# Kernel optimization log

Measured on AMD Instinct MI355X. Metric: run time of the kernel, lower is better.

The kernel has to match this reference:

```python
import jax, jax.numpy as jnp
import numpy as np

DIM, K, B, H, W = 256, 7, 16, 56, 56
EPS = 1e-5

def _conv(x, w, pad, groups=1):
    return jax.lax.conv_general_dilated(
        x, w, window_strides=(1, 1), padding=[(pad, pad), (pad, pad)],
        dimension_numbers=('NCHW', 'OIHW', 'NCHW'), feature_group_count=groups)

def _bn(x, g, b, m, v):
    scale = g / jnp.sqrt(v + EPS)          # [C]
    bias = b - m * scale
    return x * scale[None, :, None, None] + bias[None, :, None, None]

def _silu(x):
    return x * jax.nn.sigmoid(x)

def setup_inputs() -> dict:
    key = jax.random.key(0)
    ks = jax.random.split(key, 12)
    f = lambda k_, shp, s=0.05: jax.random.normal(k_, shp, jnp.float32) * s
    d = {
        'x':   jax.random.normal(ks[0], (B, DIM, H, W), jnp.float32),
        # RepConv branch: dense 3x3 conv + BN, dense 1x1 conv + BN
        'w3':  f(ks[1], (DIM, DIM, 3, 3)),
        'g1':  1.0 + f(ks[2], (DIM,)), 'b1': f(ks[3], (DIM,)),
        'm1':  f(ks[4], (DIM,)),       'v1': jax.random.uniform(ks[4], (DIM,), jnp.float32) + 0.5,
        'w1':  f(ks[5], (DIM, DIM, 1, 1)),
        'g2':  1.0 + f(ks[6], (DIM,)), 'b2': f(ks[7], (DIM,)),
        'm2':  f(ks[8], (DIM,)),       'v2': jax.random.uniform(ks[8], (DIM,), jnp.float32) + 0.5,
        # depthwise branches
        'dw7': f(ks[9], (DIM, 1, 7, 7)),
        'dwk': f(ks[10], (DIM, 1, K, K)),
        # final BN
        'g3':  1.0 + f(ks[11], (DIM,)), 'b3': f(ks[11], (DIM,)),
        'm3':  f(ks[11], (DIM,)),       'v3': jax.random.uniform(ks[11], (DIM,), jnp.float32) + 0.5,
    }
    return d

def reference(x, w3, g1, b1, m1, v1, w1, g2, b2, m2, v2, dw7, dwk, g3, b3, m3, v3):
    # RepConv (train-mode, bn=False): SiLU(BN(conv3x3(x)) + BN(conv1x1(x)))
    rep = _silu(_bn(_conv(x, w3, 1), g1, b1, m1, v1)
                + _bn(_conv(x, w1, 0), g2, b2, m2, v2))
    # parallel depthwise branches
    y = rep + _conv(x, dw7, 3, groups=DIM) + _conv(x, dwk, K // 2, groups=DIM)
    return _silu(_bn(y, g3, b3, m3, v3))
```

## Files before the change

kernel.cpp:

```cpp
#include <hip/hip_runtime.h>
#include <stdint.h>
#include <stddef.h>

#define DIM 256
#define NB 16
#define HH 56
#define WW 56
#define HWP (HH*WW)
#define PH 62
#define PW 62
#define NPIX (NB*HWP)
#define EPSV 1e-5f

using f32x4  = __attribute__((ext_vector_type(4))) float;
using bf16x8 = __attribute__((ext_vector_type(8))) __bf16;

static __device__ __forceinline__ unsigned short f2bf(float f) {
    union { float f; unsigned u; } v; v.f = f;
    unsigned r = v.u + 0x7FFFu + ((v.u >> 16) & 1u);
    return (unsigned short)(r >> 16);
}
static __device__ __forceinline__ float bf2f(unsigned short u) {
    union { unsigned u; float f; } v; v.u = ((unsigned)u) << 16; return v.f;
}
static __device__ __forceinline__ float silu_f(float z) {
    return z / (1.f + __expf(-z));
}

__global__ __launch_bounds__(256)
void fused_prep(const float* __restrict__ x,
                const float* __restrict__ w3, const float* __restrict__ g1,
                const float* __restrict__ b1, const float* __restrict__ m1,
                const float* __restrict__ v1, const float* __restrict__ w1,
                const float* __restrict__ g2, const float* __restrict__ b2,
                const float* __restrict__ m2, const float* __restrict__ v2,
                const float* __restrict__ dw7, const float* __restrict__ dwk,
                const float* __restrict__ g3, const float* __restrict__ b3,
                const float* __restrict__ m3, const float* __restrict__ v3,
                unsigned short* __restrict__ xpad, unsigned short* __restrict__ WkT,
                unsigned short* __restrict__ dwout, float* __restrict__ biasm,
                float* __restrict__ sc3, float* __restrict__ bi3)
{
    __shared__ float shbuf[PH*64];
    int bid = blockIdx.x;
    int t = threadIdx.x;

    if (bid < 4096) {
        float (*plane)[64] = (float(*)[64])shbuf;
        int c = bid & 255, b = bid >> 8;
#pragma unroll
        for (int j = 0; j < 4; ++j) {
            int idx = j*256 + t;
            if (idx < 992) ((f32x4*)plane)[idx] = (f32x4){0.f,0.f,0.f,0.f};
        }
        __syncthreads();
        const float* xp = x + ((size_t)b*DIM + c)*HWP;
#pragma unroll
        for (int j = 0; j < 13; ++j) {
            int idx = j*256 + t;
            if (idx < HWP) {
                int h = idx / 56, w = idx % 56;
                plane[h + 3][w + 3] = xp[idx];
            }
        }
        float wr[49];
#pragma unroll
        for (int i = 0; i < 49; ++i) wr[i] = dw7[c*49 + i] + dwk[c*49 + i];
        __syncthreads();
        unsigned short* op = dwout + ((size_t)b*DIM + c)*HWP;
#pragma unroll
        for (int j = 0; j < 2; ++j) {
            int q = j*256 + t;
            if (q < 392) {
                int h = q / 7, w0 = (q % 7)*8;
                float a[8] = {0.f,0.f,0.f,0.f,0.f,0.f,0.f,0.f};
#pragma unroll
                for (int dy = 0; dy < 7; ++dy) {
                    const float* row = &plane[h + dy][w0];
                    union { f32x4 v[4]; float s[16]; } rr;
                    rr.v[0] = *(const f32x4*)(row);
                    rr.v[1] = *(const f32x4*)(row + 4);
                    rr.v[2] = *(const f32x4*)(row + 8);
                    rr.v[3] = *(const f32x4*)(row + 12);
#pragma unroll
                    for (int dx = 0; dx < 7; ++dx) {
                        float wv = wr[dy*7 + dx];
#pragma unroll
                        for (int o = 0; o < 8; ++o) a[o] += rr.s[dx + o] * wv;
                    }
                }
                uint4 pk;
                pk.x = (unsigned)f2bf(a[0]) | ((unsigned)f2bf(a[1]) << 16);
                pk.y = (unsigned)f2bf(a[2]) | ((unsigned)f2bf(a[3]) << 16);
                pk.z = (unsigned)f2bf(a[4]) | ((unsigned)f2bf(a[5]) << 16);
                pk.w = (unsigned)f2bf(a[6]) | ((unsigned)f2bf(a[7]) << 16);
                *(uint4*)&op[h*WW + w0] = pk;
            }
        }
        return;
    }

    if (bid < 8064) {
        float (*lds)[57] = (float(*)[57])shbuf;
        int idx0 = bid - 4096;
        int cc = idx0 & 3;
        int r62 = (idx0 >> 2);
        int ph = r62 % PH, b = r62 / PH;
        int c0 = cc*64;
        char* rowc = (char*)xpad + ((size_t)(b*PH + ph)*PW)*(DIM*2) + c0*2;

        if (ph < 3 || ph >= HH + 3) {
            uint4 z = {0u,0u,0u,0u};
#pragma unroll
            for (int j = 0; j < 2; ++j) {
                int idx = j*256 + t;
                if (idx < 496) {
                    int pix = idx >> 3, q = idx & 7;
                    *(uint4*)(rowc + (size_t)pix*(DIM*2) + q*16) = z;
                }
            }
            return;
        }
        if (t < 48) {
            int p = t >> 3, q = t & 7;
            int pw = (p < 3) ? p : (PW - 6 + p);
            uint4 z = {0u,0u,0u,0u};
            *(uint4*)(rowc + (size_t)pw*(DIM*2) + q*16) = z;
        }
        int h = ph - 3;
#pragma unroll
        for (int j = 0; j < 14; ++j) {
            int idx = j*256 + t;
            int c = idx / 56, w = idx % 56;
            lds[c][w] = x[((size_t)(b*DIM + c0 + c)*HH + h)*WW + w];
        }
        __syncthreads();
#pragma unroll
        for (int j = 0; j < 7; ++j) {
            int idx = j*256 + t;
            int w = idx >> 5, cp = idx & 31;
            unsigned lo = f2bf(lds[2*cp][w]);
            unsigned hi = f2bf(lds[2*cp+1][w]);
            unsigned val = lo | (hi << 16);
            *(unsigned*)(rowc + (size_t)(w + 3)*(DIM*2) + 4*cp) = val;
        }
        return;
    }

    {
        int co = bid - 8064;
        float s1 = g1[co] * rsqrtf(v1[co] + EPSV);
        float s2 = g2[co] * rsqrtf(v2[co] + EPSV);
        float w1v = w1[co*DIM + t] * s2;
        const float* w3r = w3 + (size_t)(co*DIM + t)*9;
#pragma unroll
        for (int s = 0; s < 9; ++s) {
            float v = w3r[s]*s1 + (s == 4 ? w1v : 0.f);
            WkT[((size_t)s*DIM + co)*DIM + t] = f2bf(v);
        }
        if (t == 0) {
            biasm[co] = (b1[co] - m1[co]*s1) + (b2[co] - m2[co]*s2);
            float s3 = g3[co] * rsqrtf(v3[co] + EPSV);
            sc3[co] = s3;
            bi3[co] = b3[co] - m3[co]*s3;
        }
    }
}

__global__ __launch_bounds__(256, 2)
void main_conv(const unsigned short* __restrict__ xpad, const unsigned short* __restrict__ WkT,
               const unsigned short* __restrict__ dwo, const float* __restrict__ biasm,
               const float* __restrict__ sc3, const float* __restrict__ bi3,
               float* __restrict__ out)
{
    __shared__ __align__(16) char smem[65536];
    int t = threadIdx.x;
    int lane = t & 63, wv = t >> 6;
    int wm = wv >> 1, wn = wv & 1;
    int qm = lane & 15, qg = lane >> 4;
    int bx = blockIdx.y;
    int byc = blockIdx.x;

    int swz = (((lane & 7) ^ ((lane >> 3) & 7)) << 4);

    uintptr_t gA[4], gB[4];
#pragma unroll
    for (int r = 0; r < 4; ++r) {
        int pixt = r*32 + wv*8 + (lane >> 3);
        int P = bx*128 + pixt;
        int bb = P / HWP, rem = P % HWP;
        int h = rem / WW, w = rem % WW;
        gA[r] = (uintptr_t)xpad + ((size_t)((bb*PH + h + 2)*PW + (w + 2))*DIM)*2 + swz;
        int cog = byc*128 + pixt;
        gB[r] = (uintptr_t)WkT + ((size_t)cog*DIM)*2 + swz;
    }

    f32x4 acc[4][4] = {};

    auto stage = [&](int s, int buf) {
        int ch = s / 9, tap = s - ch*9;
        int ky = tap / 3, kx = tap - ky*3;
        int offA = (ky*PW + kx)*(DIM*2) + ch*128;
        int offB = tap*(DIM*DIM*2) + ch*128;
        char* base = smem + buf*32768;
#pragma unroll
        for (int r = 0; r < 4; ++r) {
            __builtin_amdgcn_global_load_lds(
                (const __attribute__((address_space(1))) void*)(gA[r] + offA),
                (__attribute__((address_space(3))) void*)(base + (r*32 + wv*8)*128),
                16, 0, 0);
            __builtin_amdgcn_global_load_lds(
                (const __attribute__((address_space(1))) void*)(gB[r] + offB),
                (__attribute__((address_space(3))) void*)(base + 16384 + (r*32 + wv*8)*128),
                16, 0, 0);
        }
    };

    int kxo = (qg << 4) ^ ((lane & 7) << 4);
    auto compute = [&](int buf) {
        const char* pA = smem + buf*32768 + (wm*64 + qm)*128;
        const char* pB = smem + buf*32768 + 16384 + (wn*64 + qm)*128;
#pragma unroll
        for (int kk = 0; kk < 2; ++kk) {
            int ko = kxo ^ (kk << 6);
            bf16x8 a[4], b[4];
#pragma unroll
            for (int i = 0; i < 4; ++i) {
                a[i] = *(const bf16x8*)(pA + i*2048 + ko);
                b[i] = *(const bf16x8*)(pB + i*2048 + ko);
            }
#pragma unroll
            for (int i = 0; i < 4; ++i)
#pragma unroll
                for (int j = 0; j < 4; ++j)
                    acc[i][j] = __builtin_amdgcn_mfma_f32_16x16x32_bf16(a[i], b[j], acc[i][j], 0, 0, 0);
        }
    };

    stage(0, 0);
    __syncthreads();
#pragma unroll 1
    for (int it = 0; it < 18; ++it) {
        stage(2*it + 1, 1);
        compute(0);
        __syncthreads();
        if (it < 17) stage(2*it + 2, 0);
        compute(1);
        __syncthreads();
    }

    float* ep = (float*)smem + wv*1088;
#pragma unroll
    for (int mi = 0; mi < 4; ++mi) {
#pragma unroll
        for (int ni = 0; ni < 4; ++ni)
#pragma unroll
            for (int r = 0; r < 4; ++r)
                ep[(ni*16 + qm)*17 + 4*qg + r] = acc[mi][ni][r];
        __syncthreads();
        int P = bx*128 + wm*64 + mi*16 + qm;
        int bb = P / HWP, rem = P % HWP;
        size_t obase = (size_t)bb*DIM*HWP + rem;
#pragma unroll
        for (int j = 0; j < 16; ++j) {
            int col = j*4 + qg;
            int cog = byc*128 + wn*64 + col;
            float z = ep[col*17 + qm] + biasm[cog];
            float rep = silu_f(z);
            float y = rep + bf2f(dwo[obase + (size_t)cog*HWP]);
            float yy = y * sc3[cog] + bi3[cog];
            out[obase + (size_t)cog*HWP] = silu_f(yy);
        }
        __syncthreads();
    }
}

extern "C" void kernel_launch(void* const* d_in, const int* in_sizes, int n_in,
                              void* d_out, int out_size, void* d_ws, size_t ws_size,
                              hipStream_t stream)
{
    (void)in_sizes; (void)n_in; (void)out_size; (void)ws_size;
    const float* x   = (const float*)d_in[0];
    const float* w3  = (const float*)d_in[1];
    const float* g1  = (const float*)d_in[2];
    const float* b1  = (const float*)d_in[3];
    const float* m1  = (const float*)d_in[4];
    const float* v1  = (const float*)d_in[5];
    const float* w1  = (const float*)d_in[6];
    const float* g2  = (const float*)d_in[7];
    const float* b2  = (const float*)d_in[8];
    const float* m2  = (const float*)d_in[9];
    const float* v2  = (const float*)d_in[10];
    const float* dw7 = (const float*)d_in[11];
    const float* dwk = (const float*)d_in[12];
    const float* g3  = (const float*)d_in[13];
    const float* b3  = (const float*)d_in[14];
    const float* m3  = (const float*)d_in[15];
    const float* v3  = (const float*)d_in[16];
    float* out = (float*)d_out;

    char* ws = (char*)d_ws;
    unsigned short* xpad = (unsigned short*)(ws);
    unsigned short* WkT  = (unsigned short*)(ws + 31490048);
    unsigned short* dwo  = (unsigned short*)(ws + 32669696);
    float* biasm = (float*)(ws + 58359808);
    float* sc3   = (float*)(ws + 58360832);
    float* bi3   = (float*)(ws + 58361856);

    fused_prep<<<dim3(8320), dim3(256), 0, stream>>>(
        x, w3, g1, b1, m1, v1, w1, g2, b2, m2, v2, dw7, dwk, g3, b3, m3, v3,
        xpad, WkT, dwo, biasm, sc3, bi3);
    main_conv<<<dim3(2, NPIX/128), dim3(256), 0, stream>>>(xpad, WkT, dwo, biasm, sc3, bi3, out);
}
```

Baseline: 143.5 us.

## Single-buffer LDS staging to raise occupancy to four blocks per CU

The main implicit-GEMM conv kernel now uses one 32KB LDS buffer instead of a double buffer and asks for four blocks per CU in launch bounds instead of two. Each k-step loads the tile, waits on vmcnt(0), hits a barrier, computes and hits another barrier, so loads no longer overlap MFMA within a block. The idea is to hide latency through more resident waves across blocks rather than software pipelining, at the cost of exposed load latency per block and a tighter register budget that could cause spills.

```diff
diff --git a/kernel.cpp b/kernel.cpp
--- a/kernel.cpp
+++ b/kernel.cpp
@@ -167,13 +167,13 @@
     }
 }
 
-__global__ __launch_bounds__(256, 2)
+__global__ __launch_bounds__(256, 4)
 void main_conv(const unsigned short* __restrict__ xpad, const unsigned short* __restrict__ WkT,
                const unsigned short* __restrict__ dwo, const float* __restrict__ biasm,
                const float* __restrict__ sc3, const float* __restrict__ bi3,
                float* __restrict__ out)
 {
-    __shared__ __align__(16) char smem[65536];
+    __shared__ __align__(16) char smem[32768];
     int t = threadIdx.x;
     int lane = t & 63, wv = t >> 6;
     int wm = wv >> 1, wn = wv & 1;
@@ -197,29 +197,28 @@
 
     f32x4 acc[4][4] = {};
 
-    auto stage = [&](int s, int buf) {
+    auto stage = [&](int s) {
         int ch = s / 9, tap = s - ch*9;
         int ky = tap / 3, kx = tap - ky*3;
         int offA = (ky*PW + kx)*(DIM*2) + ch*128;
         int offB = tap*(DIM*DIM*2) + ch*128;
-        char* base = smem + buf*32768;
 #pragma unroll
         for (int r = 0; r < 4; ++r) {
             __builtin_amdgcn_global_load_lds(
                 (const __attribute__((address_space(1))) void*)(gA[r] + offA),
-                (__attribute__((address_space(3))) void*)(base + (r*32 + wv*8)*128),
+                (__attribute__((address_space(3))) void*)(smem + (r*32 + wv*8)*128),
                 16, 0, 0);
             __builtin_amdgcn_global_load_lds(
                 (const __attribute__((address_space(1))) void*)(gB[r] + offB),
-                (__attribute__((address_space(3))) void*)(base + 16384 + (r*32 + wv*8)*128),
+                (__attribute__((address_space(3))) void*)(smem + 16384 + (r*32 + wv*8)*128),
                 16, 0, 0);
         }
     };
 
     int kxo = (qg << 4) ^ ((lane & 7) << 4);
-    auto compute = [&](int buf) {
-        const char* pA = smem + buf*32768 + (wm*64 + qm)*128;
-        const char* pB = smem + buf*32768 + 16384 + (wn*64 + qm)*128;
+    auto compute = [&]() {
+        const char* pA = smem + (wm*64 + qm)*128;
+        const char* pB = smem + 16384 + (wn*64 + qm)*128;
 #pragma unroll
         for (int kk = 0; kk < 2; ++kk) {
             int ko = kxo ^ (kk << 6);
@@ -237,17 +236,18 @@
         }
     };
 
-    stage(0, 0);
-    __syncthreads();
+#define VMW0() asm volatile("s_waitcnt vmcnt(0)" ::: "memory")
+#define BARX() { asm volatile("" ::: "memory"); __builtin_amdgcn_s_barrier(); asm volatile("" ::: "memory"); }
+
 #pragma unroll 1
-    for (int it = 0; it < 18; ++it) {
-        stage(2*it + 1, 1);
-        compute(0);
-        __syncthreads();
-        if (it < 17) stage(2*it + 2, 0);
-        compute(1);
-        __syncthreads();
-    }
+    for (int s = 0; s < 36; ++s) {
+        stage(s);
+        VMW0(); BARX();
+        compute();
+        BARX();
+    }
+#undef VMW0
+#undef BARX
 
     float* ep = (float*)smem + wv*1088;
 #pragma unroll
```

New measurement: 137.0 us. -4.5%, faster.
